# Performance work log

Measured on AMD Instinct MI355X. Metric: run time of the kernel, lower is better.

## Reference

```python
import jax, jax.numpy as jnp
import numpy as np

SIZE = 1024
CODE_DIM = 256
B, H, W = 32, 32, 32


def setup_inputs() -> dict:
    key = jax.random.key(0)
    k1, k2 = jax.random.split(key)
    z = jax.random.normal(k1, (B, CODE_DIM, H, W), dtype=jnp.float32)
    embeddings = jax.random.normal(k2, (SIZE, CODE_DIM), dtype=jnp.float32)
    return {"z": z, "embeddings": embeddings}


def reference(z, embeddings):
    b, c, h, w = z.shape  # c == code_dim
    # (b, h, w, c) -> (N, c)
    flat = jnp.transpose(z, (0, 2, 3, 1)).reshape(-1, c)
    d = (
        jnp.sum(flat * flat, axis=-1, keepdims=True)
        - 2.0 * (flat @ embeddings.T)
        + jnp.sum(embeddings * embeddings, axis=-1)
    )
    idx = jnp.argmin(d, axis=-1)  # (N,)
    quantized = embeddings[idx].reshape(b, h, w, c)
    quantized = jnp.transpose(quantized, (0, 3, 1, 2))  # (b, c, h, w)
    straight_through = jax.lax.stop_gradient(quantized - z) + z
    return quantized, straight_through, idx.reshape(b, h, w)
```

## Files before the change

### kernel.cpp

```cpp
#include <hip/hip_runtime.h>

#define NPTS   32768
#define NCODES 1024
#define DIM    256
#define HWSZ   1024
#define CHW    (DIM*HWSZ)
#define QSZ    8388608

typedef __attribute__((ext_vector_type(8))) short short8;
typedef __attribute__((ext_vector_type(4))) float f32x4;

__device__ __forceinline__ void gload16(const void* g, void* l) {
    __builtin_amdgcn_global_load_lds((const __attribute__((address_space(1))) void*)g,
                                     (__attribute__((address_space(3))) void*)l,
                                     16, 0, 0);
}

__device__ __forceinline__ unsigned bf16_rne(float f) {
    unsigned u = __float_as_uint(f);
    return (u + 0x7fffu + ((u >> 16) & 1u)) >> 16;
}

__global__ void k_e2(const float* __restrict__ emb, float* __restrict__ e2) {
    int tid  = threadIdx.x;
    int lane = tid & 63;
    int w    = tid >> 6;
    int k    = blockIdx.x * 4 + w;
    const float4 v = *reinterpret_cast<const float4*>(emb + k * DIM + lane * 4);
    double s = (double)v.x * v.x + (double)v.y * v.y + (double)v.z * v.z + (double)v.w * v.w;
    #pragma unroll
    for (int m = 32; m >= 1; m >>= 1) s += __shfl_xor(s, m);
    if (lane == 0) e2[k] = (float)s;
}

__global__ void k_prep_e(const float* __restrict__ emb, short* __restrict__ Eh,
                         short* __restrict__ El) {
    int idx = blockIdx.x * 256 + threadIdx.x;
    float4 v = reinterpret_cast<const float4*>(emb)[idx];
    float f[4] = {v.x, v.y, v.z, v.w};
    short h[4], l[4];
    #pragma unroll
    for (int i = 0; i < 4; ++i) {
        unsigned hb = bf16_rne(f[i]);
        float hf = __uint_as_float(hb << 16);
        h[i] = (short)hb;
        l[i] = (short)bf16_rne(f[i] - hf);
    }
    reinterpret_cast<short4*>(Eh)[idx] = make_short4(h[0], h[1], h[2], h[3]);
    reinterpret_cast<short4*>(El)[idx] = make_short4(l[0], l[1], l[2], l[3]);
}

__global__ void k_prep_x(const float* __restrict__ z, short* __restrict__ Xh,
                         short* __restrict__ Xl) {
    __shared__ float T[64][65];
    int blk = blockIdx.x;
    int b   = blk >> 6;
    int ct  = (blk >> 4) & 3;
    int ht  = blk & 15;
    int c0 = ct * 64, hw0 = ht * 64;
    int tid = threadIdx.x;
    int cc = tid & 63, r0 = tid >> 6;
    const float* zp = z + b * CHW;
    #pragma unroll
    for (int i = 0; i < 16; ++i) {
        int r = r0 + i * 4;
        T[r][cc] = zp[(c0 + r) * HWSZ + hw0 + cc];
    }
    __syncthreads();
    int cl = tid & 63;
    #pragma unroll
    for (int i = 0; i < 16; ++i) {
        int hwl = r0 + i * 4;
        float f = T[cl][hwl];
        unsigned hb = bf16_rne(f);
        float hf = __uint_as_float(hb << 16);
        unsigned lb = bf16_rne(f - hf);
        int n = b * HWSZ + hw0 + hwl;
        Xh[n * DIM + c0 + cl] = (short)hb;
        Xl[n * DIM + c0 + cl] = (short)lb;
    }
}

__launch_bounds__(256, 2)
__global__ void k_dist(const short* __restrict__ Xh, const short* __restrict__ Xl,
                       const short* __restrict__ Eh, const short* __restrict__ El,
                       const float* __restrict__ e2, float* __restrict__ minv,
                       int* __restrict__ mini) {
    __shared__ __align__(16) short As[4096];
    __shared__ __align__(16) short Bs[4096];
    __shared__ float sv[2][128];
    __shared__ int   si[2][128];

    const int tid = threadIdx.x;
    const int ct = blockIdx.x & 7;
    const int pt = blockIdx.x >> 3;
    const int n0 = pt * 128;
    const int c0 = ct * 128;

    const int w = tid >> 6, lane = tid & 63;
    const int wr = w >> 1, wc = w & 1;
    const int m16 = lane & 15, quad = lane >> 4;

    f32x4 acc[4][4];
    #pragma unroll
    for (int i = 0; i < 4; ++i)
        #pragma unroll
        for (int j = 0; j < 4; ++j) acc[i][j] = (f32x4){0.f, 0.f, 0.f, 0.f};

    const int row = tid >> 2;
    const int ks  = (tid & 3) * 8;

    char* aDst0 = (char*)As + w * 1024;
    char* aDst1 = (char*)As + 4096 + w * 1024;
    char* bDst0 = (char*)Bs + w * 1024;
    char* bDst1 = (char*)Bs + 4096 + w * 1024;

    for (int t = 0; t < 24; ++t) {
        const int seg  = t >> 3;
        const int koff = (t & 7) * 32 + ks;
        const short* Asrc = (seg == 2) ? Xl : Xh;
        const short* Bsrc = (seg == 1) ? El : Eh;
        __syncthreads();
        gload16(Asrc + (n0 + row) * DIM + koff,      aDst0);
        gload16(Asrc + (n0 + 64 + row) * DIM + koff, aDst1);
        gload16(Bsrc + (c0 + row) * DIM + koff,      bDst0);
        gload16(Bsrc + (c0 + 64 + row) * DIM + koff, bDst1);
        __syncthreads();

        short8 af[4], bf[4];
        #pragma unroll
        for (int i = 0; i < 4; ++i)
            af[i] = *(const short8*)&As[(wr * 64 + i * 16 + m16) * 32 + quad * 8];
        #pragma unroll
        for (int j = 0; j < 4; ++j)
            bf[j] = *(const short8*)&Bs[(wc * 64 + j * 16 + m16) * 32 + quad * 8];
        #pragma unroll
        for (int i = 0; i < 4; ++i)
            #pragma unroll
            for (int j = 0; j < 4; ++j)
                acc[i][j] = __builtin_amdgcn_mfma_f32_16x16x32_bf16(af[i], bf[j], acc[i][j], 0, 0, 0);
    }

    float ecol[4];
    #pragma unroll
    for (int j = 0; j < 4; ++j) ecol[j] = e2[c0 + wc * 64 + j * 16 + m16];

    #pragma unroll
    for (int i = 0; i < 4; ++i) {
        #pragma unroll
        for (int r = 0; r < 4; ++r) {
            float best = 3.4e38f; int bi = 0;
            #pragma unroll
            for (int j = 0; j < 4; ++j) {
                float d = fmaf(-2.f, acc[i][j][r], ecol[j]);
                int code = c0 + wc * 64 + j * 16 + m16;
                if (d < best) { best = d; bi = code; }
            }
            #pragma unroll
            for (int m = 1; m < 16; m <<= 1) {
                float ov = __shfl_xor(best, m);
                int   oi = __shfl_xor(bi, m);
                if (ov < best || (ov == best && oi < bi)) { best = ov; bi = oi; }
            }
            if (m16 == 0) {
                int p = wr * 64 + i * 16 + quad * 4 + r;
                sv[wc][p] = best; si[wc][p] = bi;
            }
        }
    }
    __syncthreads();
    if (tid < 128) {
        float v0 = sv[0][tid]; int i0 = si[0][tid];
        float v1 = sv[1][tid]; int i1 = si[1][tid];
        if (v1 < v0) { v0 = v1; i0 = i1; }
        minv[ct * NPTS + n0 + tid] = v0;
        mini[ct * NPTS + n0 + tid] = i0;
    }
}

__global__ void k_argmin(const float* __restrict__ minv, const int* __restrict__ mini,
                         int* __restrict__ idxw, float* __restrict__ idxf) {
    int n = blockIdx.x * 256 + threadIdx.x;
    float bv = minv[n]; int bi = mini[n];
    #pragma unroll
    for (int g = 1; g < 8; ++g) {
        float v = minv[g * NPTS + n]; int ii = mini[g * NPTS + n];
        if (v < bv) { bv = v; bi = ii; }
    }
    idxw[n] = bi;
    idxf[n] = (float)bi;
}

__global__ void k_out2(const float* __restrict__ z, const float* __restrict__ emb,
                       const int* __restrict__ idx, float* __restrict__ out) {
    int tid = threadIdx.x;
    int n  = blockIdx.x * 32 + (tid & 31);
    int ch = tid >> 5;
    int bi = idx[n];
    int b = n >> 10, hw = n & 1023;
    const float* ep = emb + bi * DIM + ch * 32;
    int base = b * CHW + (ch * 32) * HWSZ + hw;
    #pragma unroll 8
    for (int c = 0; c < 32; ++c) {
        float ev = ep[c];
        int off = base + c * HWSZ;
        float zv = z[off];
        out[off] = ev;
        out[QSZ + off] = (ev - zv) + zv;
    }
}

extern "C" void kernel_launch(void* const* d_in, const int* in_sizes, int n_in,
                              void* d_out, int out_size, void* d_ws, size_t ws_size,
                              hipStream_t stream) {
    const float* z   = (const float*)d_in[0];
    const float* emb = (const float*)d_in[1];
    float* out = (float*)d_out;
    float* ws  = (float*)d_ws;

    short* Eh   = (short*)ws;
    short* El   = (short*)(ws + 131072);
    float* e2   = ws + 262144;
    float* minv = ws + 263168;
    int*   mini = (int*)(ws + 525312);
    int*   idxw = (int*)(ws + 787456);

    short* Xh = (short*)out;
    short* Xl = (short*)(out + 4194304);
    float* idxf = out + 2 * QSZ;

    hipLaunchKernelGGL(k_prep_e, dim3(256),  dim3(256), 0, stream, emb, Eh, El);
    hipLaunchKernelGGL(k_e2,     dim3(256),  dim3(256), 0, stream, emb, e2);
    hipLaunchKernelGGL(k_prep_x, dim3(2048), dim3(256), 0, stream, z, Xh, Xl);
    hipLaunchKernelGGL(k_dist,   dim3(2048), dim3(256), 0, stream, Xh, Xl, Eh, El, e2, minv, mini);
    hipLaunchKernelGGL(k_argmin, dim3(128),  dim3(256), 0, stream, minv, mini, idxw, idxf);
    hipLaunchKernelGGL(k_out2,   dim3(1024), dim3(256), 0, stream, z, emb, idxw, out);
}
```

Before: 190.0 us.

## Fuse prep/argmin/output kernels and load hi/lo tiles together in distance GEMM

Merges the e2 norm computation into the embedding split kernel and folds the cross-tile argmin into a vectorized output kernel that writes float4 rows. In the distance kernel, each k-step now loads the high and low bf16 tiles for both operands at once and issues all three split-precision MFMA passes. This cuts the main loop from 24 to 8 iterations and halves barrier count per MFMA. The block order is also remapped so consecutive blocks share an embedding tile, and launch bounds ask for 3 blocks per SM. The cost is double the LDS, more fragment registers, and possible occupancy pressure.

After: 190.4 us. About the same (+0.2%).

```diff
diff --git a/kernel.cpp b/kernel.cpp
--- a/kernel.cpp
+++ b/kernel.cpp
@@ -21,33 +21,27 @@
     return (u + 0x7fffu + ((u >> 16) & 1u)) >> 16;
 }
 
-__global__ void k_e2(const float* __restrict__ emb, float* __restrict__ e2) {
-    int tid  = threadIdx.x;
-    int lane = tid & 63;
-    int w    = tid >> 6;
-    int k    = blockIdx.x * 4 + w;
+__global__ void k_prep_e(const float* __restrict__ emb, short* __restrict__ Eh,
+                         short* __restrict__ El, float* __restrict__ e2) {
+    int tid = threadIdx.x, lane = tid & 63, w = tid >> 6;
+    int k = blockIdx.x * 4 + w;
     const float4 v = *reinterpret_cast<const float4*>(emb + k * DIM + lane * 4);
-    double s = (double)v.x * v.x + (double)v.y * v.y + (double)v.z * v.z + (double)v.w * v.w;
-    #pragma unroll
-    for (int m = 32; m >= 1; m >>= 1) s += __shfl_xor(s, m);
-    if (lane == 0) e2[k] = (float)s;
-}
-
-__global__ void k_prep_e(const float* __restrict__ emb, short* __restrict__ Eh,
-                         short* __restrict__ El) {
-    int idx = blockIdx.x * 256 + threadIdx.x;
-    float4 v = reinterpret_cast<const float4*>(emb)[idx];
     float f[4] = {v.x, v.y, v.z, v.w};
     short h[4], l[4];
+    double s = 0.0;
     #pragma unroll
     for (int i = 0; i < 4; ++i) {
         unsigned hb = bf16_rne(f[i]);
         float hf = __uint_as_float(hb << 16);
         h[i] = (short)hb;
         l[i] = (short)bf16_rne(f[i] - hf);
-    }
-    reinterpret_cast<short4*>(Eh)[idx] = make_short4(h[0], h[1], h[2], h[3]);
-    reinterpret_cast<short4*>(El)[idx] = make_short4(l[0], l[1], l[2], l[3]);
+        s += (double)f[i] * f[i];
+    }
+    *reinterpret_cast<short4*>(Eh + k * DIM + lane * 4) = make_short4(h[0], h[1], h[2], h[3]);
+    *reinterpret_cast<short4*>(El + k * DIM + lane * 4) = make_short4(l[0], l[1], l[2], l[3]);
+    #pragma unroll
+    for (int m = 32; m >= 1; m >>= 1) s += __shfl_xor(s, m);
+    if (lane == 0) e2[k] = (float)s;
 }
 
 __global__ void k_prep_x(const float* __restrict__ z, short* __restrict__ Xh,
@@ -81,19 +75,21 @@
     }
 }
 
-__launch_bounds__(256, 2)
+__launch_bounds__(256, 3)
 __global__ void k_dist(const short* __restrict__ Xh, const short* __restrict__ Xl,
                        const short* __restrict__ Eh, const short* __restrict__ El,
                        const float* __restrict__ e2, float* __restrict__ minv,
                        int* __restrict__ mini) {
-    __shared__ __align__(16) short As[4096];
-    __shared__ __align__(16) short Bs[4096];
+    __shared__ __align__(16) short Ah[4096];
+    __shared__ __align__(16) short Al[4096];
+    __shared__ __align__(16) short Bh[4096];
+    __shared__ __align__(16) short Bl[4096];
     __shared__ float sv[2][128];
     __shared__ int   si[2][128];
 
     const int tid = threadIdx.x;
-    const int ct = blockIdx.x & 7;
-    const int pt = blockIdx.x >> 3;
+    const int pt = blockIdx.x & 255;
+    const int ct = blockIdx.x >> 8;
     const int n0 = pt * 128;
     const int c0 = ct * 128;
 
@@ -107,38 +103,56 @@
         #pragma unroll
         for (int j = 0; j < 4; ++j) acc[i][j] = (f32x4){0.f, 0.f, 0.f, 0.f};
 
-    const int row = tid >> 2;
-    const int ks  = (tid & 3) * 8;
-
-    char* aDst0 = (char*)As + w * 1024;
-    char* aDst1 = (char*)As + 4096 + w * 1024;
-    char* bDst0 = (char*)Bs + w * 1024;
-    char* bDst1 = (char*)Bs + 4096 + w * 1024;
-
-    for (int t = 0; t < 24; ++t) {
-        const int seg  = t >> 3;
-        const int koff = (t & 7) * 32 + ks;
-        const short* Asrc = (seg == 2) ? Xl : Xh;
-        const short* Bsrc = (seg == 1) ? El : Eh;
+    const int r  = lane >> 2;
+    const int ks = (lane & 3) * 8;
+    const int ldsoff0 = (w * 16) * 64;
+    const int ldsoff1 = (64 + w * 16) * 64;
+    const int arow0 = (n0 + w * 16 + r) * DIM;
+    const int arow1 = (n0 + 64 + w * 16 + r) * DIM;
+    const int brow0 = (c0 + w * 16 + r) * DIM;
+    const int brow1 = (c0 + 64 + w * 16 + r) * DIM;
+
+    for (int t = 0; t < 8; ++t) {
+        const int koff = t * 32 + ks;
         __syncthreads();
-        gload16(Asrc + (n0 + row) * DIM + koff,      aDst0);
-        gload16(Asrc + (n0 + 64 + row) * DIM + koff, aDst1);
-        gload16(Bsrc + (c0 + row) * DIM + koff,      bDst0);
-        gload16(Bsrc + (c0 + 64 + row) * DIM + koff, bDst1);
+        gload16(Xh + arow0 + koff, (char*)Ah + ldsoff0);
+        gload16(Xh + arow1 + koff, (char*)Ah + ldsoff1);
+        gload16(Xl + arow0 + koff, (char*)Al + ldsoff0);
+        gload16(Xl + arow1 + koff, (char*)Al + ldsoff1);
+        gload16(Eh + brow0 + koff, (char*)Bh + ldsoff0);
+        gload16(Eh + brow1 + koff, (char*)Bh + ldsoff1);
+        gload16(El + brow0 + koff, (char*)Bl + ldsoff0);
+        gload16(El + brow1 + koff, (char*)Bl + ldsoff1);
         __syncthreads();
 
-        short8 af[4], bf[4];
+        short8 ah[4], al[4], bh[4], bl[4];
+        #pragma unroll
+        for (int i = 0; i < 4; ++i) {
+            int ar = (wr * 64 + i * 16 + m16) * 32 + quad * 8;
+            ah[i] = *(const short8*)&Ah[ar];
+            al[i] = *(const short8*)&Al[ar];
+        }
+        #pragma unroll
+        for (int j = 0; j < 4; ++j) {
+            int br = (wc * 64 + j * 16 + m16) * 32 + quad * 8;
+            bh[j] = *(const short8*)&Bh[br];
+            bl[j] = *(const short8*)&Bl[br];
+        }
         #pragma unroll
         for (int i = 0; i < 4; ++i)
-            af[i] = *(const short8*)&As[(wr * 64 + i * 16 + m16) * 32 + quad * 8];
-        #pragma unroll
-        for (int j = 0; j < 4; ++j)
-            bf[j] = *(const short8*)&Bs[(wc * 64 + j * 16 + m16) * 32 + quad * 8];
+            #pragma unroll
+            for (int j = 0; j < 4; ++j)
+                acc[i][j] = __builtin_amdgcn_mfma_f32_16x16x32_bf16(ah[i], bh[j], acc[i][j], 0, 0, 0);
         #pragma unroll
         for (int i = 0; i < 4; ++i)
             #pragma unroll
             for (int j = 0; j < 4; ++j)
-                acc[i][j] = __builtin_amdgcn_mfma_f32_16x16x32_bf16(af[i], bf[j], acc[i][j], 0, 0, 0);
+                acc[i][j] = __builtin_amdgcn_mfma_f32_16x16x32_bf16(al[i], bh[j], acc[i][j], 0, 0, 0);
+        #pragma unroll
+        for (int i = 0; i < 4; ++i)
+            #pragma unroll
+            for (int j = 0; j < 4; ++j)
+                acc[i][j] = __builtin_amdgcn_mfma_f32_16x16x32_bf16(ah[i], bl[j], acc[i][j], 0, 0, 0);
     }
 
     float ecol[4];
@@ -148,11 +162,11 @@
     #pragma unroll
     for (int i = 0; i < 4; ++i) {
         #pragma unroll
-        for (int r = 0; r < 4; ++r) {
+        for (int rr = 0; rr < 4; ++rr) {
             float best = 3.4e38f; int bi = 0;
             #pragma unroll
             for (int j = 0; j < 4; ++j) {
-                float d = fmaf(-2.f, acc[i][j][r], ecol[j]);
+                float d = fmaf(-2.f, acc[i][j][rr], ecol[j]);
                 int code = c0 + wc * 64 + j * 16 + m16;
                 if (d < best) { best = d; bi = code; }
             }
@@ -163,7 +177,7 @@
                 if (ov < best || (ov == best && oi < bi)) { best = ov; bi = oi; }
             }
             if (m16 == 0) {
-                int p = wr * 64 + i * 16 + quad * 4 + r;
+                int p = wr * 64 + i * 16 + quad * 4 + rr;
                 sv[wc][p] = best; si[wc][p] = bi;
             }
         }
@@ -178,35 +192,39 @@
     }
 }
 
-__global__ void k_argmin(const float* __restrict__ minv, const int* __restrict__ mini,
-                         int* __restrict__ idxw, float* __restrict__ idxf) {
-    int n = blockIdx.x * 256 + threadIdx.x;
-    float bv = minv[n]; int bi = mini[n];
-    #pragma unroll
-    for (int g = 1; g < 8; ++g) {
-        float v = minv[g * NPTS + n]; int ii = mini[g * NPTS + n];
-        if (v < bv) { bv = v; bi = ii; }
-    }
-    idxw[n] = bi;
-    idxf[n] = (float)bi;
-}
-
-__global__ void k_out2(const float* __restrict__ z, const float* __restrict__ emb,
-                       const int* __restrict__ idx, float* __restrict__ out) {
+__global__ void k_out(const float* __restrict__ z, const float* __restrict__ emb,
+                      const float* __restrict__ minv, const int* __restrict__ mini,
+                      float* __restrict__ out) {
+    __shared__ int sbi[64];
+    int n0 = blockIdx.x * 64;
     int tid = threadIdx.x;
-    int n  = blockIdx.x * 32 + (tid & 31);
-    int ch = tid >> 5;
-    int bi = idx[n];
-    int b = n >> 10, hw = n & 1023;
-    const float* ep = emb + bi * DIM + ch * 32;
-    int base = b * CHW + (ch * 32) * HWSZ + hw;
-    #pragma unroll 8
-    for (int c = 0; c < 32; ++c) {
-        float ev = ep[c];
-        int off = base + c * HWSZ;
-        float zv = z[off];
-        out[off] = ev;
-        out[QSZ + off] = (ev - zv) + zv;
+    if (tid < 64) {
+        int n = n0 + tid;
+        float bv = minv[n]; int bi = mini[n];
+        #pragma unroll
+        for (int g = 1; g < 8; ++g) {
+            float v = minv[g * NPTS + n]; int ii = mini[g * NPTS + n];
+            if (v < bv) { bv = v; bi = ii; }
+        }
+        sbi[tid] = bi;
+        out[2 * QSZ + n] = (float)bi;
+    }
+    __syncthreads();
+    int hwq = tid & 15, cb = tid >> 4;
+    int b = n0 >> 10, hw0 = (n0 & 1023) + hwq * 4;
+    const float* ep0 = emb + sbi[hwq * 4 + 0] * DIM;
+    const float* ep1 = emb + sbi[hwq * 4 + 1] * DIM;
+    const float* ep2 = emb + sbi[hwq * 4 + 2] * DIM;
+    const float* ep3 = emb + sbi[hwq * 4 + 3] * DIM;
+    #pragma unroll 4
+    for (int c = cb; c < DIM; c += 16) {
+        int off = b * CHW + c * HWSZ + hw0;
+        float4 zv = *reinterpret_cast<const float4*>(z + off);
+        float4 q = make_float4(ep0[c], ep1[c], ep2[c], ep3[c]);
+        *reinterpret_cast<float4*>(out + off) = q;
+        float4 st = make_float4((q.x - zv.x) + zv.x, (q.y - zv.y) + zv.y,
+                                (q.z - zv.z) + zv.z, (q.w - zv.w) + zv.w);
+        *reinterpret_cast<float4*>(out + QSZ + off) = st;
     }
 }
 
@@ -223,16 +241,12 @@
     float* e2   = ws + 262144;
     float* minv = ws + 263168;
     int*   mini = (int*)(ws + 525312);
-    int*   idxw = (int*)(ws + 787456);
 
     short* Xh = (short*)out;
     short* Xl = (short*)(out + 4194304);
-    float* idxf = out + 2 * QSZ;
-
-    hipLaunchKernelGGL(k_prep_e, dim3(256),  dim3(256), 0, stream, emb, Eh, El);
-    hipLaunchKernelGGL(k_e2,     dim3(256),  dim3(256), 0, stream, emb, e2);
+
+    hipLaunchKernelGGL(k_prep_e, dim3(256),  dim3(256), 0, stream, emb, Eh, El, e2);
     hipLaunchKernelGGL(k_prep_x, dim3(2048), dim3(256), 0, stream, z, Xh, Xl);
     hipLaunchKernelGGL(k_dist,   dim3(2048), dim3(256), 0, stream, Xh, Xl, Eh, El, e2, minv, mini);
-    hipLaunchKernelGGL(k_argmin, dim3(128),  dim3(256), 0, stream, minv, mini, idxw, idxf);
-    hipLaunchKernelGGL(k_out2,   dim3(1024), dim3(256), 0, stream, z, emb, idxw, out);
-}
+    hipLaunchKernelGGL(k_out,    dim3(512),  dim3(256), 0, stream, z, emb, minv, mini, out);
+}
```
